# Optimization experiments

Hardware: AMD Instinct MI355X
Metric: run time of the kernel (lower is better)

## Reference

```python
import jax, jax.numpy as jnp
import numpy as np

PRECS = 1e-05
# HBV parameter scaling bounds (order: BETA, FC, K0, K1, K2, LP, PERC, UZL, TT, CFMAX, CFR, CWH, BETAET)
LB = jnp.array([1.0, 50.0, 0.05, 0.01, 0.001, 0.2, 0.0, 0.0, -2.5, 0.5, 0.0, 0.0, 0.3], dtype=jnp.float32)
UB = jnp.array([6.0, 1000.0, 0.9, 0.5, 0.2, 1.0, 10.0, 100.0, 2.5, 10.0, 0.1, 0.2, 5.0], dtype=jnp.float32)

NSTEP, NGRID, MU = 730, 1000, 8

def setup_inputs() -> dict:
    key = jax.random.key(0)
    k1, k2, k3, k4 = jax.random.split(key, 4)
    P = jax.random.uniform(k1, (NSTEP, NGRID), jnp.float32) * 10.0      # precip mm/day
    T = jax.random.normal(k2, (NSTEP, NGRID), jnp.float32) * 8.0 + 2.0  # temp degC
    ET = jax.random.uniform(k3, (NSTEP, NGRID), jnp.float32) * 5.0      # PET mm/day
    x = jnp.stack([P, T, ET], axis=-1)                                   # [Nstep, Ngrid, 3]
    parameters = jax.random.uniform(k4, (NSTEP, NGRID, 13, MU), jnp.float32)  # raw in [0,1]
    tdlst = jnp.arange(2, dtype=jnp.int32)  # -> param indices {12, 0} = BETAET, BETA dynamic
    return {"x": x, "parameters": parameters, "staind": NSTEP - 1, "tdlst": tdlst, "mu": MU}

def _hbv_forward(x, parameters, staind, tdlst):
    # scale raw params to physical ranges: [Nstep, Ngrid, 13, mu]
    parT = LB[None, None, :, None] + parameters * (UB - LB)[None, None, :, None]
    # static params taken from time index staind, broadcast over time
    parhbv = jnp.broadcast_to(parT[staind][None], parT.shape)
    # dynamic params: dydrop=0 -> bernoulli mask is all zeros -> comPar = dynPar
    idx = jnp.mod(jnp.asarray(tdlst) - 1, 13)
    parhbv = parhbv.at[:, :, idx, :].set(parT[:, :, idx, :])

    Ngrid = x.shape[1]
    mu = parameters.shape[-1]
    init = tuple(jnp.full((Ngrid, mu), 0.001, dtype=jnp.float32) for _ in range(5))

    def step(carry, inp):
        SP, MW, SM, SUZ, SLZ = carry
        P_, T_, ET_, par = inp              # P_/T_/ET_: [Ngrid], par: [Ngrid, 13, mu]
        P_, T_, ET_ = P_[:, None], T_[:, None], ET_[:, None]
        BETA, FC, K0, K1, K2, LP, PERCc, UZL, TT, CFMAX, CFR, CWH, BETAET = (
            par[:, i] for i in range(13))
        is_rain = (T_ >= TT).astype(jnp.float32)
        RAIN = P_ * is_rain
        SNOW = P_ * (1.0 - is_rain)
        SP = SP + SNOW
        melt = jnp.minimum(jnp.maximum(CFMAX * (T_ - TT), 0.0), SP)
        MW = MW + melt
        SP = SP - melt
        refr = jnp.minimum(jnp.maximum(CFR * CFMAX * (TT - T_), 0.0), MW)
        SP = SP + refr
        MW = MW - refr
        tosoil = jnp.maximum(MW - CWH * SP, 0.0)
        MW = MW - tosoil
        soil_wetness = jnp.clip((SM / FC) ** BETA, 0.0, 1.0)
        recharge = (RAIN + tosoil) * soil_wetness
        SM = SM + RAIN + tosoil - recharge
        excess = jnp.maximum(SM - FC, 0.0)
        SM = SM - excess
        evapfactor = jnp.clip((SM / (LP * FC)) ** BETAET, 0.0, 1.0)
        ETact = jnp.minimum(SM, ET_ * evapfactor)
        SM = jnp.maximum(SM - ETact, PRECS)
        SUZ = SUZ + recharge + excess
        PERC = jnp.minimum(SUZ, PERCc)
        SUZ = SUZ - PERC
        Q0 = K0 * jnp.maximum(SUZ - UZL, 0.0)
        SUZ = SUZ - Q0
        Q1 = K1 * SUZ
        SUZ = SUZ - Q1
        SLZ = SLZ + PERC
        Q2 = K2 * SLZ
        SLZ = SLZ - Q2
        return (SP, MW, SM, SUZ, SLZ), Q0 + Q1 + Q2

    _, Qsimmu = jax.lax.scan(step, init, (x[:, :, 0], x[:, :, 1], x[:, :, 2], parhbv))
    # muwts=None -> mean over components; routOpt=False -> Qs = Qsimave[..., None]
    return Qsimmu.mean(-1)[..., None]  # [Nstep, Ngrid, 1]

def reference(x, parameters, staind, tdlst, mu):
    return _hbv_forward(x, parameters, staind, tdlst)
```

## Files before the change

### kernel.cpp

```cpp
#include <hip/hip_runtime.h>

#define NSTEP 730
#define NGRID 1000
#define NPAR  13
#define PRECS 1e-5f

#define PAR_TSTRIDE 104000u
#define PAR_GSTRIDE 104u
#define X_TSTRIDE 3000u

#define G10   10
#define NG10  73

#define GSTEPS 10
#define NGROUP 73

constexpr float LB_[NPAR] = {1.0f, 50.0f, 0.05f, 0.01f, 0.001f, 0.2f, 0.0f,
                             0.0f, -2.5f, 0.5f, 0.0f, 0.0f, 0.3f};
constexpr float UB_[NPAR] = {6.0f, 1000.0f, 0.9f, 0.5f, 0.2f, 1.0f, 10.0f,
                             100.0f, 2.5f, 10.0f, 0.1f, 0.2f, 5.0f};

__device__ __forceinline__ float fast_rcp(float x)  { return __builtin_amdgcn_rcpf(x); }
__device__ __forceinline__ float fast_exp2(float x) { return __builtin_amdgcn_exp2f(x); }
__device__ __forceinline__ float fast_log2(float x) { return __builtin_amdgcn_logf(x); }

__device__ __forceinline__ int mod13(int v) {
    int r = v % NPAR;
    if (r < 0) r += NPAR;
    return r;
}

template <int CTRL>
__device__ __forceinline__ float dpp_xadd(float v) {
    int r = __builtin_amdgcn_update_dpp(0, __float_as_int(v), CTRL, 0xF, 0xF, true);
    return v + __int_as_float(r);
}
__device__ __forceinline__ float mu8_sum(float v) {
    v = dpp_xadd<0xB1>(v);
    v = dpp_xadd<0x4E>(v);
    int s = __builtin_amdgcn_ds_swizzle(__float_as_int(v), 0x101F);
    return v + __int_as_float(s);
}
__device__ __forceinline__ float mu8_sum_dpp(float v) {
    v = dpp_xadd<0xB1>(v);
    v = dpp_xadd<0x4E>(v);
    v = dpp_xadd<0x141>(v);
    return v;
}

__device__ __forceinline__ float hbv_step_core(
    float P_, float T_, float ET_,
    float BETA, float FC, float K0, float K1, float K2,
    float PERCc, float UZL, float TT, float CFMAX, float CFR, float CWH,
    float BETAET, float rcpFC, float rcpLPFC,
    float& SP, float& MW, float& SM, float& SUZ, float& SLZ)
{
    float dT    = T_ - TT;
    float RAIN  = (T_ >= TT) ? P_ : 0.f;
    float SNOW  = P_ - RAIN;
    SP += SNOW;
    float cm    = CFMAX * dT;
    float melt  = fminf(fmaxf(cm, 0.f), SP);
    MW += melt; SP -= melt;
    float refr  = fminf(fmaxf(-CFR * cm, 0.f), MW);
    SP += refr; MW -= refr;
    float tosoil = fmaxf(MW - CWH * SP, 0.f);
    MW -= tosoil;
    float soilw  = fminf(fast_exp2(BETA * fast_log2(SM * rcpFC)), 1.f);
    float rt     = RAIN + tosoil;
    float rech   = rt * soilw;
    SM += rt - rech;
    float excess = fmaxf(SM - FC, 0.f);
    SM -= excess;
    float evapf  = fminf(fast_exp2(BETAET * fast_log2(SM * rcpLPFC)), 1.f);
    float ETact  = fminf(SM, ET_ * evapf);
    SM = fmaxf(SM - ETact, PRECS);
    SUZ += rech + excess;
    float PERC = fminf(SUZ, PERCc);
    SUZ -= PERC;
    float Q0 = K0 * fmaxf(SUZ - UZL, 0.f);
    SUZ -= Q0;
    float Q1 = K1 * SUZ;
    SUZ -= Q1;
    SLZ += PERC;
    float Q2 = K2 * SLZ;
    SLZ -= Q2;
    return Q0 + Q1 + Q2;
}

__device__ void hbv_generic2(
    const float* __restrict__ x, const float* __restrict__ par,
    int staind, int idx0, int idx1, float* __restrict__ out, int g, int m)
{
    const unsigned cpar = (unsigned)g * PAR_GSTRIDE + (unsigned)m;
    const unsigned g3   = (unsigned)g * 3u;

    float lb0 = 0.f, dv0 = 0.f, lb1 = 0.f, dv1 = 0.f;
    float sel0[NPAR], sel1[NPAR];
#pragma unroll
    for (int i = 0; i < NPAR; ++i) {
        sel0[i] = (idx0 == i) ? 1.f : 0.f;
        sel1[i] = (idx1 == i && idx1 != idx0) ? 1.f : 0.f;
        if (idx0 == i) { lb0 = LB_[i]; dv0 = UB_[i] - LB_[i]; }
        if (idx1 == i) { lb1 = LB_[i]; dv1 = UB_[i] - LB_[i]; }
    }
    const unsigned off0 = (unsigned)idx0 * 8u, off1 = (unsigned)idx1 * 8u;

    float basep[NPAR];
    const unsigned sbase = (unsigned)staind * PAR_TSTRIDE + cpar;
#pragma unroll
    for (int i = 0; i < NPAR; ++i) {
        float fxv = fmaf(par[sbase + (unsigned)i * 8u], UB_[i] - LB_[i], LB_[i]);
        basep[i] = fxv * (1.f - sel0[i] - sel1[i]);
    }

    float bP[2][GSTEPS], bT[2][GSTEPS], bEv[2][GSTEPS];
    float bS0[2][GSTEPS], bS1[2][GSTEPS];
    float SP = 0.001f, MW = 0.001f, SM = 0.001f, SUZ = 0.001f, SLZ = 0.001f;

    auto load = [&](int b, int t0) {
#pragma unroll
        for (int j = 0; j < GSTEPS; ++j) {
            unsigned t  = (unsigned)(t0 + j);
            unsigned xo = t * X_TSTRIDE + g3;
            bP[b][j]  = x[xo];
            bT[b][j]  = x[xo + 1u];
            bEv[b][j] = x[xo + 2u];
            unsigned po = t * PAR_TSTRIDE + cpar;
            bS0[b][j] = par[po + off0];
            bS1[b][j] = par[po + off1];
        }
    };
    auto compute = [&](int b, int t0) {
        float ql[GSTEPS];
#pragma unroll
        for (int j = 0; j < GSTEPS; ++j) {
            float sv0 = fmaf(bS0[b][j], dv0, lb0);
            float sv1 = fmaf(bS1[b][j], dv1, lb1);
            float pr[NPAR];
#pragma unroll
            for (int i = 0; i < NPAR; ++i)
                pr[i] = fmaf(sel1[i], sv1, fmaf(sel0[i], sv0, basep[i]));
            float rcpFC   = fast_rcp(pr[1]);
            float rcpLPFC = fast_rcp(pr[5] * pr[1]);
            ql[j] = hbv_step_core(bP[b][j], bT[b][j], bEv[b][j],
                                  pr[0], pr[1], pr[2], pr[3], pr[4], pr[6],
                                  pr[7], pr[8], pr[9], pr[10], pr[11], pr[12],
                                  rcpFC, rcpLPFC, SP, MW, SM, SUZ, SLZ);
        }
#pragma unroll
        for (int j = 0; j < GSTEPS; ++j) {
            float s = mu8_sum(ql[j]);
            if (m == 0)
                out[(unsigned)(t0 + j) * (unsigned)NGRID + (unsigned)g] = s * 0.125f;
        }
    };

    load(0, 0);
    for (int gp = 0; gp < NGROUP; gp += 2) {
        if (gp + 1 < NGROUP) load(1, (gp + 1) * GSTEPS);
        compute(0, gp * GSTEPS);
        if (gp + 2 < NGROUP) load(0, (gp + 2) * GSTEPS);
        if (gp + 1 < NGROUP) compute(1, (gp + 1) * GSTEPS);
    }
}

__global__ __launch_bounds__(64, 1) void hbv_fast(
    const float* __restrict__ x, const float* __restrict__ par,
    const int* __restrict__ staind_p, const int* __restrict__ tdlst_p,
    float* __restrict__ out)
{
    const int lane  = threadIdx.x;
    const int chain = blockIdx.x * 64 + lane;
    const int g = chain >> 3;
    const int m = chain & 7;

    const int staind = __builtin_amdgcn_readfirstlane(staind_p[0]);
    const int idx0   = __builtin_amdgcn_readfirstlane(mod13(tdlst_p[0] - 1));
    const int idx1   = __builtin_amdgcn_readfirstlane(mod13(tdlst_p[1] - 1));

    if (!(idx0 == 12 && idx1 == 0)) {
        hbv_generic2(x, par, staind, idx0, idx1, out, g, m);
        return;
    }

    const unsigned cpar = (unsigned)g * PAR_GSTRIDE + (unsigned)m;
    const unsigned g3   = (unsigned)g * 3u;

    float fx[NPAR];
    const unsigned sbase = (unsigned)staind * PAR_TSTRIDE + cpar;
#pragma unroll
    for (int i = 0; i < NPAR; ++i)
        fx[i] = fmaf(par[sbase + (unsigned)i * 8u], UB_[i] - LB_[i], LB_[i]);

    const float FC = fx[1], K0 = fx[2], K1 = fx[3], K2 = fx[4],
                PERCc = fx[6], UZL = fx[7], TT = fx[8], CFMAX = fx[9],
                CWH = fx[11];
    const float CC       = fx[10] * fx[9];
    const float rcpFC    = fast_rcp(fx[1]);
    const float rcpLPFC  = fast_rcp(fx[5] * fx[1]);
    const float l2rcpFC  = fast_log2(rcpFC);
    const float l2rcpLPF = fast_log2(rcpLPFC);
    constexpr float lbB = LB_[0],  dvB = UB_[0]  - LB_[0];
    constexpr float lbE = LB_[12], dvE = UB_[12] - LB_[12];

    float vP[3][G10], vT[3][G10], vE[3][G10], v0[3][G10], v1[3][G10];

    struct F3 { float a, b, c; };

    auto gload = [&](int b, int grp) {
        const int t0 = grp * G10;
        const float* xp = x   + (unsigned)t0 * X_TSTRIDE  + g3;
        const float* pp = par + (unsigned)t0 * PAR_TSTRIDE + cpar;
#pragma unroll
        for (int j = 0; j < G10; ++j) {
            F3 xv = *reinterpret_cast<const F3*>(xp);
            vP[b][j] = xv.a; vT[b][j] = xv.b; vE[b][j] = xv.c;
            v1[b][j] = pp[0];
            v0[b][j] = pp[96];
            xp += X_TSTRIDE;
            pp += PAR_TSTRIDE;
        }
    };

    float SP = 0.001f, MW = 0.001f, SM = 0.001f, SUZ = 0.001f, SLZ = 0.001f;

    auto compute = [&](int b, int grp) {
        const int t0 = grp * G10;
#pragma unroll
        for (int j = 0; j < G10; ++j) {
            float Pj = vP[b][j], Tj = vT[b][j], ET = vE[b][j];
            float dT     = Tj - TT;
            float RAIN   = (dT >= 0.f) ? Pj : 0.f;
            float SNOW   = Pj - RAIN;
            float MAXCM  = fmaxf(CFMAX * dT, 0.f);
            float MAXRF  = fmaxf(-CC * dT, 0.f);
            float BETAET = fmaf(v0[b][j], dvE, lbE);
            float BETA   = fmaf(v1[b][j], dvB, lbB);
            float bbc    = BETA * l2rcpFC;
            float ebc    = BETAET * l2rcpLPF;

            SP += SNOW;
            float melt = fminf(MAXCM, SP);
            MW += melt; SP -= melt;
            float refr = fminf(MAXRF, MW);
            SP += refr; MW -= refr;
            float tosoil = fmaxf(fmaf(-CWH, SP, MW), 0.f);
            MW -= tosoil;
            float rt    = RAIN + tosoil;
            float soilw = fast_exp2(fmaf(BETA, fast_log2(SM), bbc));
            float rech  = rt * soilw;
            float SM_mid = SM + rt - rech;
            float SM_ae  = fminf(SM_mid, FC);
            float excess = SM_mid - SM_ae;
            float evapf  = fminf(fast_exp2(fmaf(BETAET, fast_log2(SM_ae), ebc)), 1.f);
            SM = fmaxf(fmaf(-ET, evapf, SM_ae), PRECS);
            SUZ += rech + excess;
            float PERC = fminf(SUZ, PERCc);
            float SUZp = SUZ - PERC;
            float Q0   = K0 * fmaxf(SUZp - UZL, 0.f);
            float SUZq = SUZp - Q0;
            float Q1   = K1 * SUZq;
            SUZ = SUZq - Q1;
            SLZ += PERC;
            float Q2 = K2 * SLZ;
            SLZ -= Q2;
            float q = (Q0 + Q1) + Q2;

            float s = mu8_sum_dpp(q);
            if (m == 0)
                out[(unsigned)(t0 + j) * (unsigned)NGRID + (unsigned)g]
                    = s * 0.125f;
        }
    };

    gload(0, 0); gload(1, 1); gload(2, 2);
    int k = 0;
    for (int t = 0; t < 24; ++t) {
        compute(0, k); if (k + 3 < NG10) gload(0, k + 3); ++k;
        compute(1, k); if (k + 3 < NG10) gload(1, k + 3); ++k;
        compute(2, k); if (k + 3 < NG10) gload(2, k + 3); ++k;
    }
    compute(0, 72);
}

__global__ __launch_bounds__(64, 1) void hbv_scan_generic(
    const float* __restrict__ x, const float* __restrict__ par,
    const int* __restrict__ staind_p, const int* __restrict__ tdlst_p,
    int n_td, float* __restrict__ out)
{
    const int tid = blockIdx.x * 64 + threadIdx.x;
    const int g   = tid >> 3;
    const int m   = tid & 7;
    if (g >= NGRID) return;

    const int staind    = staind_p[0];
    const unsigned cpar = (unsigned)g * PAR_GSTRIDE + (unsigned)m;
    const unsigned g3   = (unsigned)g * 3u;

    unsigned off[NPAR], st[NPAR];
#pragma unroll
    for (int i = 0; i < NPAR; ++i) {
        bool vr = false;
        for (int j = 0; j < n_td; ++j)
            if (mod13(tdlst_p[j] - 1) == i) vr = true;
        off[i] = (vr ? 0u : (unsigned)staind * PAR_TSTRIDE) + cpar + (unsigned)i * 8u;
        st[i]  = vr ? PAR_TSTRIDE : 0u;
    }

    float SP = 0.001f, MW = 0.001f, SM = 0.001f, SUZ = 0.001f, SLZ = 0.001f;
    for (int t = 0; t < NSTEP; ++t) {
        unsigned xo = (unsigned)t * X_TSTRIDE + g3;
        float P_ = x[xo], T_ = x[xo + 1u], E_ = x[xo + 2u];
        float pr[NPAR];
#pragma unroll
        for (int i = 0; i < NPAR; ++i) {
            pr[i] = fmaf(par[off[i]], UB_[i] - LB_[i], LB_[i]);
            off[i] += st[i];
        }
        float rcpFC   = fast_rcp(pr[1]);
        float rcpLPFC = fast_rcp(pr[5] * pr[1]);
        float q = hbv_step_core(P_, T_, E_, pr[0], pr[1], pr[2], pr[3], pr[4],
                                pr[6], pr[7], pr[8], pr[9], pr[10], pr[11],
                                pr[12], rcpFC, rcpLPFC, SP, MW, SM, SUZ, SLZ);
        float s = mu8_sum(q);
        if (m == 0) out[(unsigned)t * (unsigned)NGRID + (unsigned)g] = s * 0.125f;
    }
}

extern "C" void kernel_launch(void* const* d_in, const int* in_sizes, int n_in,
                              void* d_out, int out_size, void* d_ws, size_t ws_size,
                              hipStream_t stream) {
    const float* x      = (const float*)d_in[0];
    const float* par    = (const float*)d_in[1];
    const int*   staind = (const int*)d_in[2];
    const int*   tdlst  = (const int*)d_in[3];
    float*       out    = (float*)d_out;
    const int n_td = in_sizes[3];

    if (n_td == 2) {
        hbv_fast<<<125, 64, 0, stream>>>(x, par, staind, tdlst, out);
    } else {
        hbv_scan_generic<<<125, 64, 0, stream>>>(x, par, staind, tdlst,
                                                 n_td, out);
    }
}
```

Before: 450.4 us.

## Split HBV recurrence into producer/consumer waves pipelined through LDS

The single-wave kernel becomes a two-wave block. Wave 0 loads inputs and runs the snow/meltwater chain and the groundwater (SUZ/SLZ) chain. Wave 1 runs only the soil-moisture chain with its log/exp, taking and returning per-step values through double-buffered LDS, with a block barrier every 10 timesteps. This shortens each wave's serial dependency chain by overlapping independent sub-recurrences across waves, at the cost of LDS traffic, barriers and a three-stage pipeline lag.

```diff
diff --git a/kernel.cpp b/kernel.cpp
--- a/kernel.cpp
+++ b/kernel.cpp
@@ -14,6 +14,9 @@
 
 #define GSTEPS 10
 #define NGROUP 73
+
+#define LDS_PBUF  7680
+#define LDS_TOTAL 15360
 
 constexpr float LB_[NPAR] = {1.0f, 50.0f, 0.05f, 0.01f, 0.001f, 0.2f, 0.0f,
                              0.0f, -2.5f, 0.5f, 0.0f, 0.0f, 0.3f};
@@ -40,12 +43,6 @@
     v = dpp_xadd<0x4E>(v);
     int s = __builtin_amdgcn_ds_swizzle(__float_as_int(v), 0x101F);
     return v + __int_as_float(s);
-}
-__device__ __forceinline__ float mu8_sum_dpp(float v) {
-    v = dpp_xadd<0xB1>(v);
-    v = dpp_xadd<0x4E>(v);
-    v = dpp_xadd<0x141>(v);
-    return v;
 }
 
 __device__ __forceinline__ float hbv_step_core(
@@ -165,12 +162,15 @@
     }
 }
 
-__global__ __launch_bounds__(64, 1) void hbv_fast(
+__global__ __launch_bounds__(128, 1) void hbv_pc2(
     const float* __restrict__ x, const float* __restrict__ par,
     const int* __restrict__ staind_p, const int* __restrict__ tdlst_p,
     float* __restrict__ out)
 {
-    const int lane  = threadIdx.x;
+    __shared__ float lds[LDS_TOTAL];
+
+    const int lane  = threadIdx.x & 63;
+    const int wave  = threadIdx.x >> 6;
     const int chain = blockIdx.x * 64 + lane;
     const int g = chain >> 3;
     const int m = chain & 7;
@@ -180,7 +180,7 @@
     const int idx1   = __builtin_amdgcn_readfirstlane(mod13(tdlst_p[1] - 1));
 
     if (!(idx0 == 12 && idx1 == 0)) {
-        hbv_generic2(x, par, staind, idx0, idx1, out, g, m);
+        if (wave == 0) hbv_generic2(x, par, staind, idx0, idx1, out, g, m);
         return;
     }
 
@@ -193,95 +193,147 @@
     for (int i = 0; i < NPAR; ++i)
         fx[i] = fmaf(par[sbase + (unsigned)i * 8u], UB_[i] - LB_[i], LB_[i]);
 
-    const float FC = fx[1], K0 = fx[2], K1 = fx[3], K2 = fx[4],
-                PERCc = fx[6], UZL = fx[7], TT = fx[8], CFMAX = fx[9],
-                CWH = fx[11];
-    const float CC       = fx[10] * fx[9];
-    const float rcpFC    = fast_rcp(fx[1]);
-    const float rcpLPFC  = fast_rcp(fx[5] * fx[1]);
-    const float l2rcpFC  = fast_log2(rcpFC);
-    const float l2rcpLPF = fast_log2(rcpLPFC);
-    constexpr float lbB = LB_[0],  dvB = UB_[0]  - LB_[0];
-    constexpr float lbE = LB_[12], dvE = UB_[12] - LB_[12];
-
-    float vP[3][G10], vT[3][G10], vE[3][G10], v0[3][G10], v1[3][G10];
-
-    struct F3 { float a, b, c; };
-
-    auto gload = [&](int b, int grp) {
-        const int t0 = grp * G10;
-        const float* xp = x   + (unsigned)t0 * X_TSTRIDE  + g3;
-        const float* pp = par + (unsigned)t0 * PAR_TSTRIDE + cpar;
-#pragma unroll
-        for (int j = 0; j < G10; ++j) {
-            F3 xv = *reinterpret_cast<const F3*>(xp);
-            vP[b][j] = xv.a; vT[b][j] = xv.b; vE[b][j] = xv.c;
-            v1[b][j] = pp[0];
-            v0[b][j] = pp[96];
-            xp += X_TSTRIDE;
-            pp += PAR_TSTRIDE;
-        }
-    };
-
-    float SP = 0.001f, MW = 0.001f, SM = 0.001f, SUZ = 0.001f, SLZ = 0.001f;
-
-    auto compute = [&](int b, int grp) {
-        const int t0 = grp * G10;
-#pragma unroll
-        for (int j = 0; j < G10; ++j) {
-            float Pj = vP[b][j], Tj = vT[b][j], ET = vE[b][j];
-            float dT     = Tj - TT;
-            float RAIN   = (dT >= 0.f) ? Pj : 0.f;
-            float SNOW   = Pj - RAIN;
-            float MAXCM  = fmaxf(CFMAX * dT, 0.f);
-            float MAXRF  = fmaxf(-CC * dT, 0.f);
-            float BETAET = fmaf(v0[b][j], dvE, lbE);
-            float BETA   = fmaf(v1[b][j], dvB, lbB);
-            float bbc    = BETA * l2rcpFC;
-            float ebc    = BETAET * l2rcpLPF;
-
-            SP += SNOW;
-            float melt = fminf(MAXCM, SP);
-            MW += melt; SP -= melt;
-            float refr = fminf(MAXRF, MW);
-            SP += refr; MW -= refr;
-            float tosoil = fmaxf(fmaf(-CWH, SP, MW), 0.f);
-            MW -= tosoil;
-            float rt    = RAIN + tosoil;
-            float soilw = fast_exp2(fmaf(BETA, fast_log2(SM), bbc));
-            float rech  = rt * soilw;
-            float SM_mid = SM + rt - rech;
-            float SM_ae  = fminf(SM_mid, FC);
-            float excess = SM_mid - SM_ae;
-            float evapf  = fminf(fast_exp2(fmaf(BETAET, fast_log2(SM_ae), ebc)), 1.f);
-            SM = fmaxf(fmaf(-ET, evapf, SM_ae), PRECS);
-            SUZ += rech + excess;
-            float PERC = fminf(SUZ, PERCc);
-            float SUZp = SUZ - PERC;
-            float Q0   = K0 * fmaxf(SUZp - UZL, 0.f);
-            float SUZq = SUZp - Q0;
-            float Q1   = K1 * SUZq;
-            SUZ = SUZq - Q1;
-            SLZ += PERC;
-            float Q2 = K2 * SLZ;
-            SLZ -= Q2;
-            float q = (Q0 + Q1) + Q2;
-
-            float s = mu8_sum_dpp(q);
-            if (m == 0)
-                out[(unsigned)(t0 + j) * (unsigned)NGRID + (unsigned)g]
-                    = s * 0.125f;
-        }
-    };
-
-    gload(0, 0); gload(1, 1); gload(2, 2);
-    int k = 0;
-    for (int t = 0; t < 24; ++t) {
-        compute(0, k); if (k + 3 < NG10) gload(0, k + 3); ++k;
-        compute(1, k); if (k + 3 < NG10) gload(1, k + 3); ++k;
-        compute(2, k); if (k + 3 < NG10) gload(2, k + 3); ++k;
-    }
-    compute(0, 72);
+    if (wave == 0) {
+        const float TT = fx[8], CFMAX = fx[9], CWH = fx[11];
+        const float CC = fx[10] * fx[9];
+        const float K0 = fx[2], K1 = fx[3], K2 = fx[4],
+                    PERCc = fx[6], UZL = fx[7];
+        const float rcpFC    = fast_rcp(fx[1]);
+        const float rcpLPFC  = fast_rcp(fx[5] * fx[1]);
+        const float l2rcpFC  = fast_log2(rcpFC);
+        const float l2rcpLPF = fast_log2(rcpLPFC);
+        constexpr float lbB = LB_[0],  dvB = UB_[0]  - LB_[0];
+        constexpr float lbE = LB_[12], dvE = UB_[12] - LB_[12];
+
+        float vP[3][G10], vT[3][G10], vE[3][G10], v0[3][G10], v1[3][G10];
+
+        struct F3 { float a, b, c; };
+
+        auto gload = [&](int b, int grp) {
+            const int t0 = grp * G10;
+            const float* xp = x   + (unsigned)t0 * X_TSTRIDE  + g3;
+            const float* pp = par + (unsigned)t0 * PAR_TSTRIDE + cpar;
+#pragma unroll
+            for (int j = 0; j < G10; ++j) {
+                F3 xv = *reinterpret_cast<const F3*>(xp);
+                vP[b][j] = xv.a; vT[b][j] = xv.b; vE[b][j] = xv.c;
+                v1[b][j] = pp[0];
+                v0[b][j] = pp[96];
+                xp += X_TSTRIDE;
+                pp += PAR_TSTRIDE;
+            }
+        };
+
+        float SP = 0.001f, MW = 0.001f;
+        float SUZ = 0.001f, SLZ = 0.001f;
+
+        auto prep = [&](int b, int grp) {
+            float* pw = &lds[((unsigned)grp & 1u) * LDS_PBUF
+                             + (unsigned)lane * 12u];
+#pragma unroll
+            for (int j = 0; j < G10; ++j) {
+                float Pj = vP[b][j], Tj = vT[b][j];
+                float dT    = Tj - TT;
+                float RAIN  = (dT >= 0.f) ? Pj : 0.f;
+                float SNOW  = Pj - RAIN;
+                float MAXCM = fmaxf(CFMAX * dT, 0.f);
+                float MAXRF = fmaxf(-CC * dT, 0.f);
+                SP += SNOW;
+                float melt = fminf(MAXCM, SP);
+                MW += melt; SP -= melt;
+                float refr = fminf(MAXRF, MW);
+                SP += refr; MW -= refr;
+                float tosoil = fmaxf(fmaf(-CWH, SP, MW), 0.f);
+                MW -= tosoil;
+                float rt = RAIN + tosoil;
+                float BETAET = fmaf(v0[b][j], dvE, lbE);
+                float BETA   = fmaf(v1[b][j], dvB, lbB);
+                float bbc    = BETA * l2rcpFC;
+                float ebc    = BETAET * l2rcpLPF;
+                *reinterpret_cast<float4*>(pw + j * 768)
+                    = make_float4(rt, vE[b][j], bbc, ebc);
+                *reinterpret_cast<float2*>(pw + j * 768 + 4)
+                    = make_float2(BETA, BETAET);
+            }
+        };
+
+        auto rxwork = [&](int grp) {
+            const float* rb = &lds[((unsigned)grp & 1u) * LDS_PBUF
+                                   + (unsigned)lane * 12u + 6u];
+            float q[G10];
+#pragma unroll
+            for (int j = 0; j < G10; ++j) {
+                float rxv = rb[j * 768];
+                SUZ += rxv;
+                float PERC = fminf(SUZ, PERCc);
+                float SUZp = SUZ - PERC;
+                float Q0   = K0 * fmaxf(SUZp - UZL, 0.f);
+                float SUZq = SUZp - Q0;
+                float Q1   = K1 * SUZq;
+                SUZ = SUZq - Q1;
+                SLZ += PERC;
+                float Q2 = K2 * SLZ;
+                SLZ -= Q2;
+                q[j] = (Q0 + Q1) + Q2;
+            }
+#pragma unroll
+            for (int j = 0; j < G10; ++j) {
+                float s = mu8_sum(q[j]);
+                if (m == 0)
+                    out[(unsigned)(grp * G10 + j) * (unsigned)NGRID + (unsigned)g]
+                        = s * 0.125f;
+            }
+        };
+
+#define PHASEP(kk, BL, BP)                                   \
+        {                                                    \
+            __syncthreads();                                 \
+            if ((kk) + 3 < NG10) gload(BL, (kk) + 3);        \
+            if ((kk) + 1 < NG10) prep(BP, (kk) + 1);         \
+            if ((kk) >= 1) rxwork((kk) - 1);                 \
+        }
+
+        gload(0, 0); gload(1, 1); gload(2, 2);
+        prep(0, 0);
+        int k = 0;
+        for (int t = 0; t < 24; ++t) {
+            PHASEP(k, 0, 1); ++k;
+            PHASEP(k, 1, 2); ++k;
+            PHASEP(k, 2, 0); ++k;
+        }
+        PHASEP(k, 0, 1);
+        __syncthreads();
+        rxwork(72);
+#undef PHASEP
+    } else {
+        const float FC = fx[1];
+        float SM = 0.001f;
+
+        for (int k = 0; k < NG10; ++k) {
+            __syncthreads();
+            float* cb = &lds[((unsigned)k & 1u) * LDS_PBUF
+                             + (unsigned)lane * 12u];
+#pragma unroll
+            for (int j = 0; j < G10; ++j) {
+                float4 a  = *reinterpret_cast<const float4*>(cb + j * 768);
+                float2 bv = *reinterpret_cast<const float2*>(cb + j * 768 + 4);
+                float rt = a.x, ET = a.y, bbc = a.z, ebc = a.w;
+                float BETA = bv.x, BETAET = bv.y;
+
+                float soilw  = fast_exp2(fmaf(BETA, fast_log2(SM), bbc));
+                float rech   = rt * soilw;
+                float SM_mid = SM + rt - rech;
+                float SM_ae  = fminf(SM_mid, FC);
+                float excess = SM_mid - SM_ae;
+                float evapf  = fminf(
+                    fast_exp2(fmaf(BETAET, fast_log2(SM_ae), ebc)), 1.f);
+                SM = fmaxf(fmaf(-ET, evapf, SM_ae), PRECS);
+
+                cb[j * 768 + 6] = rech + excess;
+            }
+        }
+        __syncthreads();
+    }
 }
 
 __global__ __launch_bounds__(64, 1) void hbv_scan_generic(
@@ -339,7 +391,7 @@
     const int n_td = in_sizes[3];
 
     if (n_td == 2) {
-        hbv_fast<<<125, 64, 0, stream>>>(x, par, staind, tdlst, out);
+        hbv_pc2<<<125, 128, 0, stream>>>(x, par, staind, tdlst, out);
     } else {
         hbv_scan_generic<<<125, 64, 0, stream>>>(x, par, staind, tdlst,
                                                  n_td, out);
```

After: 610.9 us. +35.6%, slower.

## Interleave two independent HBV chains per thread and halve block count

Applied to the files above, without the earlier changes.

Each thread now runs two independent recurrence chains (A and B) interleaved step by step, so the dependent-latency chain of one can overlap with the other. The grid drops from 125 to 63 wavefronts, and the prefetch pipeline changes from triple-buffered 10-step groups to double-buffered 5-step groups. This trades per-chain parallelism across CUs for instruction-level parallelism within a wave. It risks higher register pressure and fewer CUs in use.

```diff
diff --git a/kernel.cpp b/kernel.cpp
--- a/kernel.cpp
+++ b/kernel.cpp
@@ -9,8 +9,8 @@
 #define PAR_GSTRIDE 104u
 #define X_TSTRIDE 3000u
 
-#define G10   10
-#define NG10  73
+#define G5    5
+#define NGRP5 146
 
 #define GSTEPS 10
 #define NGROUP 73
@@ -88,6 +88,52 @@
     return Q0 + Q1 + Q2;
 }
 
+__device__ __forceinline__ float hbv_step_fast(
+    float Pj, float Tj, float ET, float rv0 , float rv1 ,
+    float TT, float CFMAX, float CC, float CWH, float FC,
+    float K0, float K1, float K2, float PERCc, float UZL,
+    float l2rcpFC, float l2rcpLPF,
+    float& SP, float& MW, float& SM, float& SUZ, float& SLZ)
+{
+    constexpr float lbB = LB_[0],  dvB = UB_[0]  - LB_[0];
+    constexpr float lbE = LB_[12], dvE = UB_[12] - LB_[12];
+    float dT     = Tj - TT;
+    float RAIN   = (dT >= 0.f) ? Pj : 0.f;
+    float SNOW   = Pj - RAIN;
+    float MAXCM  = fmaxf(CFMAX * dT, 0.f);
+    float MAXRF  = fmaxf(-CC * dT, 0.f);
+    float BETAET = fmaf(rv0, dvE, lbE);
+    float BETA   = fmaf(rv1, dvB, lbB);
+    float bbc    = BETA * l2rcpFC;
+    float ebc    = BETAET * l2rcpLPF;
+    SP += SNOW;
+    float melt = fminf(MAXCM, SP);
+    MW += melt; SP -= melt;
+    float refr = fminf(MAXRF, MW);
+    SP += refr; MW -= refr;
+    float tosoil = fmaxf(fmaf(-CWH, SP, MW), 0.f);
+    MW -= tosoil;
+    float rt    = RAIN + tosoil;
+    float soilw = fast_exp2(fmaf(BETA, fast_log2(SM), bbc));
+    float rech  = rt * soilw;
+    float SM_mid = SM + rt - rech;
+    float SM_ae  = fminf(SM_mid, FC);
+    float excess = SM_mid - SM_ae;
+    float evapf  = fminf(fast_exp2(fmaf(BETAET, fast_log2(SM_ae), ebc)), 1.f);
+    SM = fmaxf(fmaf(-ET, evapf, SM_ae), PRECS);
+    SUZ += rech + excess;
+    float PERC = fminf(SUZ, PERCc);
+    float SUZp = SUZ - PERC;
+    float Q0   = K0 * fmaxf(SUZp - UZL, 0.f);
+    float SUZq = SUZp - Q0;
+    float Q1   = K1 * SUZq;
+    SUZ = SUZq - Q1;
+    SLZ += PERC;
+    float Q2 = K2 * SLZ;
+    SLZ -= Q2;
+    return (Q0 + Q1) + Q2;
+}
+
 __device__ void hbv_generic2(
     const float* __restrict__ x, const float* __restrict__ par,
     int staind, int idx0, int idx1, float* __restrict__ out, int g, int m)
@@ -165,123 +211,121 @@
     }
 }
 
-__global__ __launch_bounds__(64, 1) void hbv_fast(
+__global__ __launch_bounds__(64, 1) void hbv_fast3(
     const float* __restrict__ x, const float* __restrict__ par,
     const int* __restrict__ staind_p, const int* __restrict__ tdlst_p,
     float* __restrict__ out)
 {
-    const int lane  = threadIdx.x;
-    const int chain = blockIdx.x * 64 + lane;
-    const int g = chain >> 3;
-    const int m = chain & 7;
+    const int tid = blockIdx.x * 64 + threadIdx.x;
+    const int m   = threadIdx.x & 7;
+    const int gA  = tid >> 3;
+    const bool validB = (tid < 3968);
+    const int chainB  = validB ? tid + 4032 : 7999;
+    const int gB  = chainB >> 3;
+    const int mB  = chainB & 7;
 
     const int staind = __builtin_amdgcn_readfirstlane(staind_p[0]);
     const int idx0   = __builtin_amdgcn_readfirstlane(mod13(tdlst_p[0] - 1));
     const int idx1   = __builtin_amdgcn_readfirstlane(mod13(tdlst_p[1] - 1));
 
     if (!(idx0 == 12 && idx1 == 0)) {
-        hbv_generic2(x, par, staind, idx0, idx1, out, g, m);
+        hbv_generic2(x, par, staind, idx0, idx1, out, gA, m);
+        if (validB) hbv_generic2(x, par, staind, idx0, idx1, out, gB, mB);
         return;
     }
 
-    const unsigned cpar = (unsigned)g * PAR_GSTRIDE + (unsigned)m;
-    const unsigned g3   = (unsigned)g * 3u;
-
-    float fx[NPAR];
-    const unsigned sbase = (unsigned)staind * PAR_TSTRIDE + cpar;
-#pragma unroll
-    for (int i = 0; i < NPAR; ++i)
-        fx[i] = fmaf(par[sbase + (unsigned)i * 8u], UB_[i] - LB_[i], LB_[i]);
-
-    const float FC = fx[1], K0 = fx[2], K1 = fx[3], K2 = fx[4],
-                PERCc = fx[6], UZL = fx[7], TT = fx[8], CFMAX = fx[9],
-                CWH = fx[11];
-    const float CC       = fx[10] * fx[9];
-    const float rcpFC    = fast_rcp(fx[1]);
-    const float rcpLPFC  = fast_rcp(fx[5] * fx[1]);
-    const float l2rcpFC  = fast_log2(rcpFC);
-    const float l2rcpLPF = fast_log2(rcpLPFC);
-    constexpr float lbB = LB_[0],  dvB = UB_[0]  - LB_[0];
-    constexpr float lbE = LB_[12], dvE = UB_[12] - LB_[12];
-
-    float vP[3][G10], vT[3][G10], vE[3][G10], v0[3][G10], v1[3][G10];
-
-    struct F3 { float a, b, c; };
-
-    auto gload = [&](int b, int grp) {
-        const int t0 = grp * G10;
-        const float* xp = x   + (unsigned)t0 * X_TSTRIDE  + g3;
-        const float* pp = par + (unsigned)t0 * PAR_TSTRIDE + cpar;
-#pragma unroll
-        for (int j = 0; j < G10; ++j) {
-            F3 xv = *reinterpret_cast<const F3*>(xp);
-            vP[b][j] = xv.a; vT[b][j] = xv.b; vE[b][j] = xv.c;
-            v1[b][j] = pp[0];
-            v0[b][j] = pp[96];
-            xp += X_TSTRIDE;
-            pp += PAR_TSTRIDE;
-        }
-    };
-
-    float SP = 0.001f, MW = 0.001f, SM = 0.001f, SUZ = 0.001f, SLZ = 0.001f;
-
-    auto compute = [&](int b, int grp) {
-        const int t0 = grp * G10;
-#pragma unroll
-        for (int j = 0; j < G10; ++j) {
-            float Pj = vP[b][j], Tj = vT[b][j], ET = vE[b][j];
-            float dT     = Tj - TT;
-            float RAIN   = (dT >= 0.f) ? Pj : 0.f;
-            float SNOW   = Pj - RAIN;
-            float MAXCM  = fmaxf(CFMAX * dT, 0.f);
-            float MAXRF  = fmaxf(-CC * dT, 0.f);
-            float BETAET = fmaf(v0[b][j], dvE, lbE);
-            float BETA   = fmaf(v1[b][j], dvB, lbB);
-            float bbc    = BETA * l2rcpFC;
-            float ebc    = BETAET * l2rcpLPF;
-
-            SP += SNOW;
-            float melt = fminf(MAXCM, SP);
-            MW += melt; SP -= melt;
-            float refr = fminf(MAXRF, MW);
-            SP += refr; MW -= refr;
-            float tosoil = fmaxf(fmaf(-CWH, SP, MW), 0.f);
-            MW -= tosoil;
-            float rt    = RAIN + tosoil;
-            float soilw = fast_exp2(fmaf(BETA, fast_log2(SM), bbc));
-            float rech  = rt * soilw;
-            float SM_mid = SM + rt - rech;
-            float SM_ae  = fminf(SM_mid, FC);
-            float excess = SM_mid - SM_ae;
-            float evapf  = fminf(fast_exp2(fmaf(BETAET, fast_log2(SM_ae), ebc)), 1.f);
-            SM = fmaxf(fmaf(-ET, evapf, SM_ae), PRECS);
-            SUZ += rech + excess;
-            float PERC = fminf(SUZ, PERCc);
-            float SUZp = SUZ - PERC;
-            float Q0   = K0 * fmaxf(SUZp - UZL, 0.f);
-            float SUZq = SUZp - Q0;
-            float Q1   = K1 * SUZq;
-            SUZ = SUZq - Q1;
-            SLZ += PERC;
-            float Q2 = K2 * SLZ;
-            SLZ -= Q2;
-            float q = (Q0 + Q1) + Q2;
-
-            float s = mu8_sum_dpp(q);
-            if (m == 0)
-                out[(unsigned)(t0 + j) * (unsigned)NGRID + (unsigned)g]
-                    = s * 0.125f;
-        }
-    };
-
-    gload(0, 0); gload(1, 1); gload(2, 2);
+    const unsigned cparA = (unsigned)gA * PAR_GSTRIDE + (unsigned)m;
+    const unsigned g3A   = (unsigned)gA * 3u;
+    const unsigned cparB = (unsigned)gB * PAR_GSTRIDE + (unsigned)mB;
+    const unsigned g3B   = (unsigned)gB * 3u;
+
+    float fxA[NPAR], fxB[NPAR];
+    {
+        const unsigned sbA = (unsigned)staind * PAR_TSTRIDE + cparA;
+        const unsigned sbB = (unsigned)staind * PAR_TSTRIDE + cparB;
+#pragma unroll
+        for (int i = 0; i < NPAR; ++i) {
+            fxA[i] = fmaf(par[sbA + (unsigned)i * 8u], UB_[i] - LB_[i], LB_[i]);
+            fxB[i] = fmaf(par[sbB + (unsigned)i * 8u], UB_[i] - LB_[i], LB_[i]);
+        }
+    }
+    const float FCa = fxA[1], K0a = fxA[2], K1a = fxA[3], K2a = fxA[4],
+                PCa = fxA[6], UZa = fxA[7], TTa = fxA[8], CFa = fxA[9],
+                CWa = fxA[11];
+    const float CCa = fxA[10] * fxA[9];
+    const float lFa = fast_log2(fast_rcp(fxA[1]));
+    const float lLa = fast_log2(fast_rcp(fxA[5] * fxA[1]));
+
+    const float FCb = fxB[1], K0b = fxB[2], K1b = fxB[3], K2b = fxB[4],
+                PCb = fxB[6], UZb = fxB[7], TTb = fxB[8], CFb = fxB[9],
+                CWb = fxB[11];
+    const float CCb = fxB[10] * fxB[9];
+    const float lFb = fast_log2(fast_rcp(fxB[1]));
+    const float lLb = fast_log2(fast_rcp(fxB[5] * fxB[1]));
+
+    float aP[2][G5], aT[2][G5], aE[2][G5], a0[2][G5], a1[2][G5];
+    float bP[2][G5], bT[2][G5], bE[2][G5], b0[2][G5], b1[2][G5];
+
+    float SPa = 0.001f, MWa = 0.001f, SMa = 0.001f, SUa = 0.001f, SLa = 0.001f;
+    float SPb = 0.001f, MWb = 0.001f, SMb = 0.001f, SUb = 0.001f, SLb = 0.001f;
+
+#define GLOAD2(BUF, grp)                                                   \
+    {                                                                      \
+        const int t0_ = (grp) * G5;                                        \
+        const float* xa_ = x   + (unsigned)t0_ * X_TSTRIDE   + g3A;        \
+        const float* pa_ = par + (unsigned)t0_ * PAR_TSTRIDE + cparA;      \
+        const float* xb_ = x   + (unsigned)t0_ * X_TSTRIDE   + g3B;        \
+        const float* pb_ = par + (unsigned)t0_ * PAR_TSTRIDE + cparB;      \
+        _Pragma("unroll")                                                  \
+        for (int j = 0; j < G5; ++j) {                                     \
+            float3 va_ = *reinterpret_cast<const float3*>(xa_);            \
+            aP[BUF][j] = va_.x; aT[BUF][j] = va_.y; aE[BUF][j] = va_.z;    \
+            a1[BUF][j] = pa_[0];                \
+            a0[BUF][j] = pa_[96];               \
+            float3 vb_ = *reinterpret_cast<const float3*>(xb_);            \
+            bP[BUF][j] = vb_.x; bT[BUF][j] = vb_.y; bE[BUF][j] = vb_.z;    \
+            b1[BUF][j] = pb_[0];                                           \
+            b0[BUF][j] = pb_[96];                                          \
+            xa_ += X_TSTRIDE; pa_ += PAR_TSTRIDE;                          \
+            xb_ += X_TSTRIDE; pb_ += PAR_TSTRIDE;                          \
+        }                                                                  \
+    }
+
+#define COMP2(BUF, grp)                                                    \
+    {                                                                      \
+        const int t0_ = (grp) * G5;                                        \
+        _Pragma("unroll")                                                  \
+        for (int j = 0; j < G5; ++j) {                                     \
+            float qa_ = hbv_step_fast(aP[BUF][j], aT[BUF][j], aE[BUF][j],  \
+                                      a0[BUF][j], a1[BUF][j],              \
+                                      TTa, CFa, CCa, CWa, FCa,             \
+                                      K0a, K1a, K2a, PCa, UZa, lFa, lLa,   \
+                                      SPa, MWa, SMa, SUa, SLa);            \
+            float qb_ = hbv_step_fast(bP[BUF][j], bT[BUF][j], bE[BUF][j],  \
+                                      b0[BUF][j], b1[BUF][j],              \
+                                      TTb, CFb, CCb, CWb, FCb,             \
+                                      K0b, K1b, K2b, PCb, UZb, lFb, lLb,   \
+                                      SPb, MWb, SMb, SUb, SLb);            \
+            float sa_ = mu8_sum_dpp(qa_);                                  \
+            float sb_ = mu8_sum_dpp(qb_);                                  \
+            const unsigned to_ = (unsigned)(t0_ + j) * (unsigned)NGRID;    \
+            if (m == 0)                                                    \
+                out[to_ + (unsigned)gA] = sa_ * 0.125f;                    \
+            if (m == 0 && validB)                                          \
+                out[to_ + (unsigned)gB] = sb_ * 0.125f;                    \
+        }                                                                  \
+    }
+
+    GLOAD2(0, 0);
     int k = 0;
-    for (int t = 0; t < 24; ++t) {
-        compute(0, k); if (k + 3 < NG10) gload(0, k + 3); ++k;
-        compute(1, k); if (k + 3 < NG10) gload(1, k + 3); ++k;
-        compute(2, k); if (k + 3 < NG10) gload(2, k + 3); ++k;
-    }
-    compute(0, 72);
+    for (int t = 0; t < 73; ++t) {
+        if (k + 1 < NGRP5) GLOAD2(1, k + 1);
+        COMP2(0, k); ++k;
+        if (k + 1 < NGRP5) GLOAD2(0, k + 1);
+        COMP2(1, k); ++k;
+    }
+#undef GLOAD2
+#undef COMP2
 }
 
 __global__ __launch_bounds__(64, 1) void hbv_scan_generic(
@@ -339,7 +383,7 @@
     const int n_td = in_sizes[3];
 
     if (n_td == 2) {
-        hbv_fast<<<125, 64, 0, stream>>>(x, par, staind, tdlst, out);
+        hbv_fast3<<<63, 64, 0, stream>>>(x, par, staind, tdlst, out);
     } else {
         hbv_scan_generic<<<125, 64, 0, stream>>>(x, par, staind, tdlst,
                                                  n_td, out);
```

New measurement: 687.0 us. +52.5%, slower.
